# Kernel tuning notes

Measured on AMD Instinct MI355X. Metric: run time of the kernel, lower is better.

Reference implementation:

```python
import jax, jax.numpy as jnp
import numpy as np

IN_FEATURES = 4096
OUT_FEATURES = 4096
GROUP_SIZE = 128
TOKENS = 8192


def setup_inputs() -> dict:
    key = jax.random.key(0)
    k1, k2, k3 = jax.random.split(key, 3)
    x = jax.random.normal(k1, (TOKENS, IN_FEATURES), dtype=jnp.float32)
    weight_packed = jax.random.randint(k2, (OUT_FEATURES, IN_FEATURES // 2), 0, 256, dtype=jnp.int32)
    num_groups = IN_FEATURES // GROUP_SIZE
    weight_scales = jax.random.uniform(k3, (OUT_FEATURES, num_groups), dtype=jnp.float32) * 0.02
    return {"x": x, "weight_packed": weight_packed, "weight_scales": weight_scales, "group_size": GROUP_SIZE}


def _dequantize_int4(packed, scales, group_size):
    # packed: [N, K//2] int (uint8 values); scales: [N, G]
    out_features = packed.shape[0]
    in_features = packed.shape[1] * 2
    low = (packed & 15) - 8   # even columns
    high = ((packed >> 4) & 15) - 8  # odd columns
    # interleave low/high along last axis -> [N, K]
    unpacked = jnp.stack([low, high], axis=-1).reshape(out_features, in_features)
    num_groups = in_features // group_size
    w = unpacked.reshape(out_features, num_groups, group_size).astype(scales.dtype)
    w = w * scales[:, :, None]  # per-group scale
    return w.reshape(out_features, in_features)


def reference(x, weight_packed, weight_scales, group_size):
    W = _dequantize_int4(weight_packed, weight_scales, group_size)  # [N, K]
    # nn.functional.linear: x @ W.T (bias=False)
    return jnp.einsum('tk,nk->tn', x, W)
```

## Files before the change

### kernel.cpp

```cpp
#include <hip/hip_runtime.h>
#include <hip/hip_bf16.h>
#include <cstdint>
#include <cstddef>

#define TOKENS 8192
#define IN_F   4096
#define OUT_F  4096

typedef __bf16 bf16;
typedef bf16  bf16x8 __attribute__((ext_vector_type(8)));
typedef float f32x4  __attribute__((ext_vector_type(4)));

__global__ void prep_kernel(const float* __restrict__ xin, bf16* __restrict__ xout,
                            const int* __restrict__ wp, const float* __restrict__ sc,
                            bf16* __restrict__ wout) {
    if (blockIdx.x < 16384) {
        size_t i = ((size_t)blockIdx.x * 256 + threadIdx.x) * 8;
        const float4* p = (const float4*)(xin + i);
        float4 a = p[0], b = p[1];
        bf16x8 r;
        r[0] = (bf16)a.x; r[1] = (bf16)a.y; r[2] = (bf16)a.z; r[3] = (bf16)a.w;
        r[4] = (bf16)b.x; r[5] = (bf16)b.y; r[6] = (bf16)b.z; r[7] = (bf16)b.w;
        *(bf16x8*)(xout + i) = r;
    } else {
        int t  = (blockIdx.x - 16384) * 256 + threadIdx.x;
        int j0 = t << 2;
        int n  = j0 >> 11;
        int g  = (j0 & 2047) >> 6;
        float s = sc[(n << 5) + g];
        int4 p = *(const int4*)(wp + j0);
        bf16x8 r;
        r[0] = (bf16)((float)((p.x & 15) - 8) * s);
        r[1] = (bf16)((float)(((p.x >> 4) & 15) - 8) * s);
        r[2] = (bf16)((float)((p.y & 15) - 8) * s);
        r[3] = (bf16)((float)(((p.y >> 4) & 15) - 8) * s);
        r[4] = (bf16)((float)((p.z & 15) - 8) * s);
        r[5] = (bf16)((float)(((p.z >> 4) & 15) - 8) * s);
        r[6] = (bf16)((float)((p.w & 15) - 8) * s);
        r[7] = (bf16)((float)(((p.w >> 4) & 15) - 8) * s);
        *(bf16x8*)(wout + ((size_t)j0 << 1)) = r;
    }
}

__global__ void gemm_kernel(const bf16* __restrict__ A, const bf16* __restrict__ B,
                            float* __restrict__ C) {
    __shared__ char smem[32768] __attribute__((aligned(128)));

    const int tid  = threadIdx.x;
    const int lane = tid & 63;
    const int w    = tid >> 6;
    const int mt   = blockIdx.x >> 5;
    const int nt   = blockIdx.x & 31;

    const char* ga[4]; const char* gb[4]; int ldsoff[4];
#pragma unroll
    for (int t = 0; t < 4; ++t) {
        int c   = (w * 4 + t) * 64 + lane;
        int row = c >> 3;
        int g   = (c & 7) ^ (row & 7);
        ga[t] = (const char*)A + (size_t)(mt * 128 + row) * (IN_F * 2) + g * 16;
        gb[t] = (const char*)B + (size_t)(nt * 128 + row) * (IN_F * 2) + g * 16;
        ldsoff[t] = (w * 4 + t) * 1024;
    }

    const int m_lane = lane & 15;
    const int quad   = lane >> 4;
    const int sw     = m_lane & 7;
    const int m0     = (w >> 1) * 64;
    const int n0     = (w & 1) * 64;

    f32x4 acc[4][4];
#pragma unroll
    for (int i = 0; i < 4; ++i)
#pragma unroll
        for (int j = 0; j < 4; ++j) acc[i][j] = (f32x4)0.0f;

    const bf16x8* pA = (const bf16x8*)smem;
    const bf16x8* pB = (const bf16x8*)(smem + 16384);

    for (int kt = 0; kt < IN_F / 64; ++kt) {
#pragma unroll
        for (int t = 0; t < 4; ++t) {
            __builtin_amdgcn_global_load_lds(
                (const __attribute__((address_space(1))) void*)(ga[t] + kt * 128),
                (__attribute__((address_space(3))) void*)(smem + ldsoff[t]), 16, 0, 0);
            __builtin_amdgcn_global_load_lds(
                (const __attribute__((address_space(1))) void*)(gb[t] + kt * 128),
                (__attribute__((address_space(3))) void*)(smem + 16384 + ldsoff[t]), 16, 0, 0);
        }
        __syncthreads();

#pragma unroll
        for (int h = 0; h < 2; ++h) {
            const int slot = (h * 4 + quad) ^ sw;
            bf16x8 af[4], bfr[4];
#pragma unroll
            for (int i = 0; i < 4; ++i)
                af[i] = pA[(m0 + i * 16 + m_lane) * 8 + slot];
#pragma unroll
            for (int j = 0; j < 4; ++j)
                bfr[j] = pB[(n0 + j * 16 + m_lane) * 8 + slot];
#pragma unroll
            for (int i = 0; i < 4; ++i)
#pragma unroll
                for (int j = 0; j < 4; ++j)
                    acc[i][j] = __builtin_amdgcn_mfma_f32_16x16x32_bf16(af[i], bfr[j], acc[i][j], 0, 0, 0);
        }
        __syncthreads();
    }

    size_t crow0 = (size_t)(mt * 128 + m0 + quad * 4) * OUT_F + nt * 128 + n0 + m_lane;
#pragma unroll
    for (int i = 0; i < 4; ++i)
#pragma unroll
        for (int r = 0; r < 4; ++r) {
            float* cp = C + crow0 + (size_t)(i * 16 + r) * OUT_F;
#pragma unroll
            for (int j = 0; j < 4; ++j) cp[j * 16] = acc[i][j][r];
        }
}

__global__ void naive_kernel(const float* __restrict__ x, const int* __restrict__ wp,
                             const float* __restrict__ sc, float* __restrict__ out) {
    int o = blockIdx.x * 256 + threadIdx.x;
    int t = o >> 12, n = o & 4095;
    const float* xr = x + (size_t)t * IN_F;
    const int*   wr = wp + (size_t)n * (IN_F / 2);
    float acc = 0.f;
    for (int g = 0; g < 32; ++g) {
        float s = sc[n * 32 + g];
        float part = 0.f;
        for (int j = 0; j < 64; ++j) {
            int p = wr[g * 64 + j];
            part += xr[g * 128 + 2 * j]     * (float)((p & 15) - 8);
            part += xr[g * 128 + 2 * j + 1] * (float)(((p >> 4) & 15) - 8);
        }
        acc += part * s;
    }
    out[o] = acc;
}

extern "C" void kernel_launch(void* const* d_in, const int* in_sizes, int n_in,
                              void* d_out, int out_size, void* d_ws, size_t ws_size,
                              hipStream_t stream) {
    const float* x  = (const float*)d_in[0];
    const int*   wp = (const int*)d_in[1];
    const float* sc = (const float*)d_in[2];
    float* out = (float*)d_out;

    const size_t xb_bytes = (size_t)TOKENS * IN_F * 2;
    const size_t wb_bytes = (size_t)OUT_F * IN_F * 2;

    if (ws_size >= xb_bytes + wb_bytes) {
        bf16* xb = (bf16*)d_ws;
        bf16* wb = (bf16*)((char*)d_ws + xb_bytes);
        prep_kernel<<<dim3(16384 + 8192), dim3(256), 0, stream>>>(x, xb, wp, sc, wb);
        gemm_kernel<<<dim3((TOKENS / 128) * (OUT_F / 128)), dim3(256), 0, stream>>>(xb, wb, out);
    } else {
        naive_kernel<<<dim3((TOKENS * OUT_F) / 256), dim3(256), 0, stream>>>(x, wp, sc, out);
    }
}
```

Before: 475.9 us.

## Enlarge GEMM tile to 256x128 and switch to 32x32x16 MFMA

```diff
diff --git a/kernel.cpp b/kernel.cpp
--- a/kernel.cpp
+++ b/kernel.cpp
@@ -8,8 +8,8 @@
 #define OUT_F  4096
 
 typedef __bf16 bf16;
-typedef bf16  bf16x8 __attribute__((ext_vector_type(8)));
-typedef float f32x4  __attribute__((ext_vector_type(4)));
+typedef bf16  bf16x8  __attribute__((ext_vector_type(8)));
+typedef float f32x16  __attribute__((ext_vector_type(16)));
 
 __global__ void prep_kernel(const float* __restrict__ xin, bf16* __restrict__ xout,
                             const int* __restrict__ wp, const float* __restrict__ sc,
@@ -42,9 +42,10 @@
     }
 }
 
-__global__ void gemm_kernel(const bf16* __restrict__ A, const bf16* __restrict__ B,
-                            float* __restrict__ C) {
-    __shared__ char smem[32768] __attribute__((aligned(128)));
+__global__ void __launch_bounds__(256, 2)
+gemm_kernel(const bf16* __restrict__ A, const bf16* __restrict__ B,
+            float* __restrict__ C) {
+    __shared__ char smem[49152] __attribute__((aligned(128)));
 
     const int tid  = threadIdx.x;
     const int lane = tid & 63;
@@ -52,72 +53,70 @@
     const int mt   = blockIdx.x >> 5;
     const int nt   = blockIdx.x & 31;
 
-    const char* ga[4]; const char* gb[4]; int ldsoff[4];
-#pragma unroll
-    for (int t = 0; t < 4; ++t) {
-        int c   = (w * 4 + t) * 64 + lane;
-        int row = c >> 3;
-        int g   = (c & 7) ^ (row & 7);
-        ga[t] = (const char*)A + (size_t)(mt * 128 + row) * (IN_F * 2) + g * 16;
-        gb[t] = (const char*)B + (size_t)(nt * 128 + row) * (IN_F * 2) + g * 16;
-        ldsoff[t] = (w * 4 + t) * 1024;
-    }
+    const int grow = tid >> 3;
+    const int gsw  = (tid & 7) ^ (grow & 7);
+    const char* gaBase = (const char*)A + ((size_t)(mt * 256 + grow) * IN_F + gsw * 8) * 2;
+    const char* gbBase = (const char*)B + ((size_t)(nt * 128 + grow) * IN_F + gsw * 8) * 2;
 
-    const int m_lane = lane & 15;
-    const int quad   = lane >> 4;
-    const int sw     = m_lane & 7;
-    const int m0     = (w >> 1) * 64;
-    const int n0     = (w & 1) * 64;
+    const int lm   = lane & 31;
+    const int half = lane >> 5;
+    const int sw   = lm & 7;
+    const int raBase = (w >> 1) * 128 + lm;
+    const int rbBase = (w & 1) * 64 + lm;
 
-    f32x4 acc[4][4];
+    f32x16 acc[4][2];
 #pragma unroll
     for (int i = 0; i < 4; ++i)
 #pragma unroll
-        for (int j = 0; j < 4; ++j) acc[i][j] = (f32x4)0.0f;
+        for (int j = 0; j < 2; ++j) acc[i][j] = (f32x16)0.0f;
 
-    const bf16x8* pA = (const bf16x8*)smem;
-    const bf16x8* pB = (const bf16x8*)(smem + 16384);
+    const bf16x8* sAv = (const bf16x8*)smem;
+    const bf16x8* sBv = (const bf16x8*)(smem + 32768);
 
     for (int kt = 0; kt < IN_F / 64; ++kt) {
+        const int kb = kt * 128;
 #pragma unroll
-        for (int t = 0; t < 4; ++t) {
+        for (int r = 0; r < 8; ++r)
             __builtin_amdgcn_global_load_lds(
-                (const __attribute__((address_space(1))) void*)(ga[t] + kt * 128),
-                (__attribute__((address_space(3))) void*)(smem + ldsoff[t]), 16, 0, 0);
+                (const __attribute__((address_space(1))) void*)(gaBase + (size_t)r * 32 * (IN_F * 2) + kb),
+                (__attribute__((address_space(3))) void*)(smem + r * 4096 + w * 1024), 16, 0, 0);
+#pragma unroll
+        for (int r = 0; r < 4; ++r)
             __builtin_amdgcn_global_load_lds(
-                (const __attribute__((address_space(1))) void*)(gb[t] + kt * 128),
-                (__attribute__((address_space(3))) void*)(smem + 16384 + ldsoff[t]), 16, 0, 0);
-        }
+                (const __attribute__((address_space(1))) void*)(gbBase + (size_t)r * 32 * (IN_F * 2) + kb),
+                (__attribute__((address_space(3))) void*)(smem + 32768 + r * 4096 + w * 1024), 16, 0, 0);
         __syncthreads();
 
 #pragma unroll
-        for (int h = 0; h < 2; ++h) {
-            const int slot = (h * 4 + quad) ^ sw;
-            bf16x8 af[4], bfr[4];
+        for (int h = 0; h < 4; ++h) {
+            const int slot = (h * 2 + half) ^ sw;
+            bf16x8 af[4], bfr[2];
 #pragma unroll
             for (int i = 0; i < 4; ++i)
-                af[i] = pA[(m0 + i * 16 + m_lane) * 8 + slot];
+                af[i] = sAv[(raBase + i * 32) * 8 + slot];
 #pragma unroll
-            for (int j = 0; j < 4; ++j)
-                bfr[j] = pB[(n0 + j * 16 + m_lane) * 8 + slot];
+            for (int j = 0; j < 2; ++j)
+                bfr[j] = sBv[(rbBase + j * 32) * 8 + slot];
 #pragma unroll
             for (int i = 0; i < 4; ++i)
 #pragma unroll
-                for (int j = 0; j < 4; ++j)
-                    acc[i][j] = __builtin_amdgcn_mfma_f32_16x16x32_bf16(af[i], bfr[j], acc[i][j], 0, 0, 0);
+                for (int j = 0; j < 2; ++j)
+                    acc[i][j] = __builtin_amdgcn_mfma_f32_32x32x16_bf16(af[i], bfr[j], acc[i][j], 0, 0, 0);
         }
         __syncthreads();
     }
 
-    size_t crow0 = (size_t)(mt * 128 + m0 + quad * 4) * OUT_F + nt * 128 + n0 + m_lane;
+    const int crowBase = mt * 256 + (w >> 1) * 128 + half * 4;
+    const int ccolBase = nt * 128 + (w & 1) * 64 + lm;
 #pragma unroll
     for (int i = 0; i < 4; ++i)
 #pragma unroll
-        for (int r = 0; r < 4; ++r) {
-            float* cp = C + crow0 + (size_t)(i * 16 + r) * OUT_F;
+        for (int j = 0; j < 2; ++j)
 #pragma unroll
-            for (int j = 0; j < 4; ++j) cp[j * 16] = acc[i][j][r];
-        }
+            for (int r = 0; r < 16; ++r) {
+                int row = crowBase + i * 32 + (r & 3) + 8 * (r >> 2);
+                C[(size_t)row * OUT_F + ccolBase + j * 32] = acc[i][j][r];
+            }
 }
 
 __global__ void naive_kernel(const float* __restrict__ x, const int* __restrict__ wp,
@@ -155,7 +154,7 @@
         bf16* xb = (bf16*)d_ws;
         bf16* wb = (bf16*)((char*)d_ws + xb_bytes);
         prep_kernel<<<dim3(16384 + 8192), dim3(256), 0, stream>>>(x, xb, wp, sc, wb);
-        gemm_kernel<<<dim3((TOKENS / 128) * (OUT_F / 128)), dim3(256), 0, stream>>>(xb, wb, out);
+        gemm_kernel<<<dim3((TOKENS / 256) * (OUT_F / 128)), dim3(256), 0, stream>>>(xb, wb, out);
     } else {
         naive_kernel<<<dim3((TOKENS * OUT_F) / 256), dim3(256), 0, stream>>>(x, wp, sc, out);
     }
```

Measured after the change: 499.0 us. +4.8%, slower.
